# Optimization experiments

Measured on AMD Instinct MI355X. Metric: run time of the kernel, lower is better.

Reference implementation:

```python
import jax, jax.numpy as jnp
import numpy as np

B, C, W, H = 8, 256, 128, 128
CR = C // 8  # squeeze channels
EPS = 1e-5   # InstanceNorm2d default eps


def _dw_conv(x, w, b, dil):
    # depthwise 3x3 dilated conv, NCHW, kernel [C,1,3,3], 'same' padding = dil
    out = jax.lax.conv_general_dilated(
        x, w, window_strides=(1, 1),
        padding=[(dil, dil), (dil, dil)],
        rhs_dilation=(dil, dil),
        dimension_numbers=("NCHW", "OIHW", "NCHW"),
        feature_group_count=x.shape[1])
    return out + b[None, :, None, None]


def setup_inputs() -> dict:
    key = jax.random.key(0)
    ks = jax.random.split(key, 9)
    s = 0.1
    return {
        "x": jax.random.normal(ks[0], (B, C, W, H), jnp.float32),
        "wq": jax.random.normal(ks[1], (C, 1, 3, 3), jnp.float32) * s,
        "bq": jax.random.normal(ks[2], (C,), jnp.float32) * s,
        "wk": jax.random.normal(ks[3], (C, 1, 3, 3), jnp.float32) * s,
        "bk": jax.random.normal(ks[4], (C,), jnp.float32) * s,
        "w_sq": jax.random.normal(ks[5], (CR, C), jnp.float32) * s,
        "b_sq": jax.random.normal(ks[6], (CR,), jnp.float32) * s,
        "w_ex": jax.random.normal(ks[7], (C, CR), jnp.float32) * s,
        "b_ex": jax.random.normal(ks[8], (C,), jnp.float32) * s,
    }


def reference(x, wq, bq, wk, bk, w_sq, b_sq, w_ex, b_ex):
    b, c, w, h = x.shape
    q = _dw_conv(x, wq, bq, 3)   # [B,C,W,H], dilation 3
    k = _dw_conv(x, wk, bk, 6)   # [B,C,W,H], dilation 6
    # per-channel QK matmul: contracts q's last dim with k's second-to-last (requires W==H)
    attn = jnp.einsum("bcij,bcjk->bcik", q, k)  # [B,C,W,H]
    # softmax over flattened spatial dims per (b, c)
    attn = jax.nn.softmax(attn.reshape(b, c, w * h), axis=-1).reshape(b, c, w, h)
    # channel global average pool of key, broadcast-multiply
    pool = jnp.mean(k, axis=(2, 3), keepdims=True)  # [B,C,1,1]
    y = attn * pool
    # 1x1 squeeze conv C -> C//8
    s = jnp.einsum("bcwh,dc->bdwh", y, w_sq) + b_sq[None, :, None, None]
    # InstanceNorm2d (no affine, biased variance over spatial dims)
    mu = jnp.mean(s, axis=(2, 3), keepdims=True)
    var = jnp.var(s, axis=(2, 3), keepdims=True)
    s = jax.nn.relu((s - mu) * jax.lax.rsqrt(var + EPS))
    # 1x1 expand conv C//8 -> C
    out = jnp.einsum("bdwh,cd->bcwh", s, w_ex) + b_ex[None, :, None, None]
    return out
```

## Files before the change

### kernel.cpp

```cpp
#include <hip/hip_runtime.h>
#include <cstdint>

#define WDIM 128
#define NPX  16384
#define XSTR 132
#define QSTR 136
#define XPAD 16
#define LDS_A_BYTES 69888

typedef __attribute__((ext_vector_type(8))) short short8;
typedef __attribute__((ext_vector_type(4))) float f32x4;

__device__ __forceinline__ float wave_max(float v) {
#pragma unroll
  for (int m = 32; m >= 1; m >>= 1) v = fmaxf(v, __shfl_xor(v, m));
  return v;
}
__device__ __forceinline__ float wave_sum(float v) {
#pragma unroll
  for (int m = 32; m >= 1; m >>= 1) v += __shfl_xor(v, m);
  return v;
}
__device__ __forceinline__ unsigned short f2bf(float f) {
  uint32_t u = __float_as_uint(f);
  return (unsigned short)((u + 0x7fff + ((u >> 16) & 1)) >> 16);
}
__device__ __forceinline__ float bf2f(unsigned short h) {
  return __uint_as_float(((uint32_t)h) << 16);
}

template <int DIL>
__device__ __forceinline__ void dw_conv32(float* acc, const float* xq, int r,
                                          int cl, const float* w9) {
#pragma unroll
  for (int dr = 0; dr < 3; ++dr) {
    int rr = r + DIL * (dr - 1);
    if ((unsigned)rr < 128u) {
      const float* rp = &xq[rr * XSTR];
#pragma unroll
      for (int dc = 0; dc < 3; ++dc) {
        float wgt = w9[dr * 3 + dc];
        const int off = DIL * (dc - 1);
#pragma unroll
        for (int i = 0; i < 32; ++i) {
          int cc = cl + 4 * i + off;
          float v = rp[cc];
          if (i <= 1 || i >= 30) v = ((unsigned)cc < 128u) ? v : 0.f;
          acc[i] = fmaf(wgt, v, acc[i]);
        }
      }
    }
  }
}

__global__ __launch_bounds__(512, 4)
void kA(const float* __restrict__ x, const float* __restrict__ wq,
        const float* __restrict__ bq, const float* __restrict__ wk,
        const float* __restrict__ bk, unsigned short* __restrict__ y) {
  extern __shared__ char smem[];
  float* xq = (float*)smem + XPAD;
  unsigned short* qb = (unsigned short*)smem;
  unsigned short* kt = (unsigned short*)(smem + 34816);
  float* red = (float*)(smem + 69632);

  const int bc = blockIdx.x;
  const int t = threadIdx.x;
  const float* __restrict__ xp = x + (size_t)bc * NPX;

#pragma unroll
  for (int it = 0; it < 8; ++it) {
    int i = (t + it * 512) * 4;
    int r = i >> 7, c = i & 127;
    *(float4*)&xq[r * XSTR + c] = *(const float4*)&xp[i];
  }

  const int ch = bc & 255;
  float wq9[9], wk9[9];
#pragma unroll
  for (int i = 0; i < 9; ++i) { wq9[i] = wq[ch * 9 + i]; wk9[i] = wk[ch * 9 + i]; }
  const float bqv = bq[ch], bkv = bk[ch];
  __syncthreads();

  const int r = t >> 2, cl = t & 3;
  float aq[32], ak[32];
#pragma unroll
  for (int i = 0; i < 32; ++i) { aq[i] = bqv; ak[i] = bkv; }
  dw_conv32<3>(aq, xq, r, cl, wq9);
  dw_conv32<6>(ak, xq, r, cl, wk9);

  float psum = 0.f;
#pragma unroll
  for (int i = 0; i < 32; ++i) psum += ak[i];

  __syncthreads();

#pragma unroll
  for (int i = 0; i < 32; ++i) {
    int c = cl + 4 * i;
    qb[r * QSTR + c] = f2bf(aq[i]);
    kt[c * QSTR + r] = f2bf(ak[i]);
  }
  __syncthreads();

  const int w = t >> 6, lane = t & 63;
  const int wr = w >> 2, wc = w & 3;
  const int r16 = lane & 15, kg = lane >> 4;
  f32x4 acc[4][2];
#pragma unroll
  for (int mi = 0; mi < 4; ++mi)
#pragma unroll
    for (int ni = 0; ni < 2; ++ni) acc[mi][ni] = (f32x4){0.f, 0.f, 0.f, 0.f};

#pragma unroll
  for (int kk = 0; kk < 4; ++kk) {
    const int kb = kk * 32 + kg * 8;
    short8 a0 = *(const short8*)&qb[(wr * 64 + 0 * 16 + r16) * QSTR + kb];
    short8 a1 = *(const short8*)&qb[(wr * 64 + 1 * 16 + r16) * QSTR + kb];
    short8 a2 = *(const short8*)&qb[(wr * 64 + 2 * 16 + r16) * QSTR + kb];
    short8 a3 = *(const short8*)&qb[(wr * 64 + 3 * 16 + r16) * QSTR + kb];
    short8 b0 = *(const short8*)&kt[(wc * 32 + 0 + r16) * QSTR + kb];
    short8 b1 = *(const short8*)&kt[(wc * 32 + 16 + r16) * QSTR + kb];
    acc[0][0] = __builtin_amdgcn_mfma_f32_16x16x32_bf16(a0, b0, acc[0][0], 0, 0, 0);
    acc[0][1] = __builtin_amdgcn_mfma_f32_16x16x32_bf16(a0, b1, acc[0][1], 0, 0, 0);
    acc[1][0] = __builtin_amdgcn_mfma_f32_16x16x32_bf16(a1, b0, acc[1][0], 0, 0, 0);
    acc[1][1] = __builtin_amdgcn_mfma_f32_16x16x32_bf16(a1, b1, acc[1][1], 0, 0, 0);
    acc[2][0] = __builtin_amdgcn_mfma_f32_16x16x32_bf16(a2, b0, acc[2][0], 0, 0, 0);
    acc[2][1] = __builtin_amdgcn_mfma_f32_16x16x32_bf16(a2, b1, acc[2][1], 0, 0, 0);
    acc[3][0] = __builtin_amdgcn_mfma_f32_16x16x32_bf16(a3, b0, acc[3][0], 0, 0, 0);
    acc[3][1] = __builtin_amdgcn_mfma_f32_16x16x32_bf16(a3, b1, acc[3][1], 0, 0, 0);
  }

  float amax = -3.402823466e38f;
#pragma unroll
  for (int mi = 0; mi < 4; ++mi)
#pragma unroll
    for (int ni = 0; ni < 2; ++ni)
#pragma unroll
      for (int j = 0; j < 4; ++j) amax = fmaxf(amax, acc[mi][ni][j]);
  amax = wave_max(amax);
  if (lane == 0) red[w] = amax;
  __syncthreads();
  float bmax = red[0];
#pragma unroll
  for (int w2 = 1; w2 < 8; ++w2) bmax = fmaxf(bmax, red[w2]);

  float es = 0.f;
#pragma unroll
  for (int mi = 0; mi < 4; ++mi)
#pragma unroll
    for (int ni = 0; ni < 2; ++ni)
#pragma unroll
      for (int j = 0; j < 4; ++j) {
        float e = __expf(acc[mi][ni][j] - bmax);
        acc[mi][ni][j] = e;
        es += e;
      }
  es = wave_sum(es);
  float ps = wave_sum(psum);
  if (lane == 0) { red[8 + w] = es; red[16 + w] = ps; }
  __syncthreads();
  float tsum = 0.f, tpool = 0.f;
#pragma unroll
  for (int w2 = 0; w2 < 8; ++w2) { tsum += red[8 + w2]; tpool += red[16 + w2]; }
  const float scale = (tpool * (1.f / 16384.f)) / tsum;

  unsigned short* __restrict__ yp = y + (size_t)bc * NPX;
#pragma unroll
  for (int mi = 0; mi < 4; ++mi)
#pragma unroll
    for (int ni = 0; ni < 2; ++ni) {
      const int col = wc * 32 + ni * 16 + r16;
#pragma unroll
      for (int j = 0; j < 4; ++j) {
        const int row = wr * 64 + mi * 16 + kg * 4 + j;
        yp[row * WDIM + col] = f2bf(acc[mi][ni][j] * scale);
      }
    }
}

__global__ __launch_bounds__(256, 2)
void kS(const unsigned short* __restrict__ y, const float* __restrict__ w_sq,
        unsigned short* __restrict__ sT, float* __restrict__ partials) {
  __shared__ unsigned short yT[64][264];
  __shared__ float red[256];
  const int t = threadIdx.x;
  const int w = t >> 6, lane = t & 63;
  const int r16 = lane & 15, kg = lane >> 4;
  const int b = blockIdx.x >> 6;
  const int chunk = blockIdx.x & 63;
  const unsigned short* __restrict__ yb = y + (size_t)b * 256 * NPX;

  short8 aw[2][8];
#pragma unroll
  for (int mt = 0; mt < 2; ++mt)
#pragma unroll
    for (int ks = 0; ks < 8; ++ks) {
      const float* p = &w_sq[(mt * 16 + r16) * 256 + ks * 32 + kg * 8];
      float4 f0 = *(const float4*)p;
      float4 f1 = *(const float4*)(p + 4);
      short8 a;
      a[0] = f2bf(f0.x); a[1] = f2bf(f0.y); a[2] = f2bf(f0.z); a[3] = f2bf(f0.w);
      a[4] = f2bf(f1.x); a[5] = f2bf(f1.y); a[6] = f2bf(f1.z); a[7] = f2bf(f1.w);
      aw[mt][ks] = a;
    }

  float ssum[8], ssq[8];
#pragma unroll
  for (int i = 0; i < 8; ++i) { ssum[i] = 0.f; ssq[i] = 0.f; }

  for (int st = 0; st < 4; ++st) {
    const int p0 = chunk * 256 + st * 64;
#pragma unroll
    for (int it = 0; it < 8; ++it) {
      const int tid = it * 4 + w;
      const int cg = tid & 3, pg = tid >> 2;
      const int c = cg * 64 + lane;
      short8 v = *(const short8*)&yb[(size_t)c * NPX + p0 + pg * 8];
#pragma unroll
      for (int j = 0; j < 8; ++j) yT[pg * 8 + j][c] = (unsigned short)v[j];
    }
    __syncthreads();

    f32x4 acc[2][4];
#pragma unroll
    for (int mi = 0; mi < 2; ++mi)
#pragma unroll
      for (int ni = 0; ni < 4; ++ni) acc[mi][ni] = (f32x4){0.f, 0.f, 0.f, 0.f};

#pragma unroll
    for (int ks = 0; ks < 8; ++ks) {
#pragma unroll
      for (int ni = 0; ni < 4; ++ni) {
        short8 bv = *(const short8*)&yT[ni * 16 + r16][ks * 32 + kg * 8];
        acc[0][ni] = __builtin_amdgcn_mfma_f32_16x16x32_bf16(aw[0][ks], bv, acc[0][ni], 0, 0, 0);
        acc[1][ni] = __builtin_amdgcn_mfma_f32_16x16x32_bf16(aw[1][ks], bv, acc[1][ni], 0, 0, 0);
      }
    }

#pragma unroll
    for (int mi = 0; mi < 2; ++mi)
#pragma unroll
      for (int ni = 0; ni < 4; ++ni) {
        const int px = p0 + ni * 16 + r16;
        ushort4 pk;
#pragma unroll
        for (int j = 0; j < 4; ++j) {
          float v = acc[mi][ni][j];
          ssum[mi * 4 + j] += v;
          ssq[mi * 4 + j] += v * v;
          ((unsigned short*)&pk)[j] = f2bf(v);
        }
        *(ushort4*)&sT[((size_t)b * NPX + px) * 32 + mi * 16 + kg * 4] = pk;
      }
    __syncthreads();
  }

#pragma unroll
  for (int i = 0; i < 8; ++i) {
    float sm = ssum[i], sq = ssq[i];
#pragma unroll
    for (int m = 8; m >= 1; m >>= 1) {
      sm += __shfl_xor(sm, m);
      sq += __shfl_xor(sq, m);
    }
    if (r16 == 0) {
      const int d = (i >> 2) * 16 + kg * 4 + (i & 3);
      red[w * 64 + d] = sm;
      red[w * 64 + 32 + d] = sq;
    }
  }
  __syncthreads();
  if (t < 64) {
    float tot = red[t] + red[64 + t] + red[128 + t] + red[192 + t];
    partials[(size_t)blockIdx.x * 64 + t] = tot;
  }
}

__global__ void kR(const float* __restrict__ partials, float* __restrict__ mu_rs) {
  const int b = blockIdx.x, d = threadIdx.x;
  float sm = 0.f, sq = 0.f;
  for (int ch = 0; ch < 64; ++ch) {
    const float* pp = &partials[(size_t)(b * 64 + ch) * 64];
    sm += pp[d];
    sq += pp[32 + d];
  }
  float m = sm * (1.f / 16384.f);
  float v = sq * (1.f / 16384.f) - m * m;
  mu_rs[b * 64 + d] = m;
  mu_rs[b * 64 + 32 + d] = rsqrtf(v + 1e-5f);
}

__global__ __launch_bounds__(256, 3)
void kO(const unsigned short* __restrict__ sT, const float* __restrict__ mu_rs,
        const float* __restrict__ w_ex, const float* __restrict__ b_ex,
        float* __restrict__ out) {
  const int t = threadIdx.x;
  const int w = t >> 6, lane = t & 63;
  const int r16 = lane & 15, kg = lane >> 4;
  const int b = blockIdx.x >> 8;
  const int p0 = (blockIdx.x & 255) * 64;
  const int c0 = w * 64;

  short8 aw[4];
  float bex[4];
#pragma unroll
  for (int mt = 0; mt < 4; ++mt) {
    const int c = c0 + mt * 16 + r16;
    const float* p = &w_ex[c * 32 + kg * 8];
    float4 f0 = *(const float4*)p;
    float4 f1 = *(const float4*)(p + 4);
    short8 a;
    a[0] = f2bf(f0.x); a[1] = f2bf(f0.y); a[2] = f2bf(f0.z); a[3] = f2bf(f0.w);
    a[4] = f2bf(f1.x); a[5] = f2bf(f1.y); a[6] = f2bf(f1.z); a[7] = f2bf(f1.w);
    aw[mt] = a;
    bex[mt] = b_ex[c0 + mt * 16 + kg * 4];
  }

  float m8[8], r8[8];
  {
    const float* mp = &mu_rs[b * 64 + kg * 8];
    const float* rp = &mu_rs[b * 64 + 32 + kg * 8];
#pragma unroll
    for (int q = 0; q < 8; ++q) { m8[q] = mp[q]; r8[q] = rp[q]; }
  }

  f32x4 acc[4][4];
#pragma unroll
  for (int mt = 0; mt < 4; ++mt)
#pragma unroll
    for (int ni = 0; ni < 4; ++ni) acc[mt][ni] = (f32x4){0.f, 0.f, 0.f, 0.f};

#pragma unroll
  for (int ni = 0; ni < 4; ++ni) {
    const int px = p0 + ni * 16 + r16;
    short8 sv = *(const short8*)&sT[((size_t)b * NPX + px) * 32 + kg * 8];
    short8 hb;
#pragma unroll
    for (int q = 0; q < 8; ++q) {
      float f = bf2f((unsigned short)sv[q]);
      float h = fmaxf((f - m8[q]) * r8[q], 0.f);
      hb[q] = f2bf(h);
    }
#pragma unroll
    for (int mt = 0; mt < 4; ++mt)
      acc[mt][ni] = __builtin_amdgcn_mfma_f32_16x16x32_bf16(aw[mt], hb, acc[mt][ni], 0, 0, 0);
  }

  float* __restrict__ ob = out + (size_t)b * 256 * NPX;
#pragma unroll
  for (int mt = 0; mt < 4; ++mt) {
#pragma unroll
    for (int j = 0; j < 4; ++j) {
      const int c = c0 + mt * 16 + kg * 4 + j;
      const float bv = b_ex[c];
#pragma unroll
      for (int ni = 0; ni < 4; ++ni) {
        const int px = p0 + ni * 16 + r16;
        ob[(size_t)c * NPX + px] = acc[mt][ni][j] + bv;
      }
    }
  }
}

extern "C" void kernel_launch(void* const* d_in, const int* in_sizes, int n_in,
                              void* d_out, int out_size, void* d_ws, size_t ws_size,
                              hipStream_t stream) {
  (void)in_sizes; (void)n_in; (void)out_size; (void)ws_size;
  const float* x    = (const float*)d_in[0];
  const float* wq   = (const float*)d_in[1];
  const float* bq   = (const float*)d_in[2];
  const float* wk   = (const float*)d_in[3];
  const float* bk   = (const float*)d_in[4];
  const float* w_sq = (const float*)d_in[5];
  const float* w_ex = (const float*)d_in[7];
  const float* b_ex = (const float*)d_in[8];
  float* out = (float*)d_out;

  unsigned short* sT = (unsigned short*)d_ws;
  float* partials = (float*)((char*)d_ws + (size_t)8 * NPX * 32 * 2);
  float* mu_rs = partials + (size_t)512 * 64;

  unsigned short* ybf = (unsigned short*)d_out;

  hipFuncSetAttribute((const void*)kA, hipFuncAttributeMaxDynamicSharedMemorySize,
                      LDS_A_BYTES);

  kA<<<2048, 512, LDS_A_BYTES, stream>>>(x, wq, bq, wk, bk, ybf);
  kS<<<512, 256, 0, stream>>>(ybf, w_sq, sT, partials);
  kR<<<8, 32, 0, stream>>>(partials, mu_rs);
  kO<<<2048, 256, 0, stream>>>(sT, mu_rs, w_ex, b_ex, out);
}
```

Measured before the change: 131.6 us.

## Restructure depthwise conv to contiguous per-thread column windows with vector LDS loads

The depthwise conv changes from strided columns (cl+4i) to each thread owning a contiguous 32-column span, processed in two halves of 16. Each input row window is loaded once with float4 LDS reads and shared across the q and k taps that use the same row, and edge masking is applied to the whole window. Weights are forced into scalar registers via readfirstlane, and q results are written to LDS as packed short8 stores. This cuts scalar LDS load count and the per-element bounds checks, at the cost of a larger live register window and possible bank conflicts on the transposed k stores.

Result: slower. 148.5 us (+12.8%).

```diff
diff --git a/kernel.cpp b/kernel.cpp
--- a/kernel.cpp
+++ b/kernel.cpp
@@ -28,29 +28,29 @@
 __device__ __forceinline__ float bf2f(unsigned short h) {
   return __uint_as_float(((uint32_t)h) << 16);
 }
-
-template <int DIL>
-__device__ __forceinline__ void dw_conv32(float* acc, const float* xq, int r,
-                                          int cl, const float* w9) {
-#pragma unroll
-  for (int dr = 0; dr < 3; ++dr) {
-    int rr = r + DIL * (dr - 1);
-    if ((unsigned)rr < 128u) {
-      const float* rp = &xq[rr * XSTR];
-#pragma unroll
-      for (int dc = 0; dc < 3; ++dc) {
-        float wgt = w9[dr * 3 + dc];
-        const int off = DIL * (dc - 1);
-#pragma unroll
-        for (int i = 0; i < 32; ++i) {
-          int cc = cl + 4 * i + off;
-          float v = rp[cc];
-          if (i <= 1 || i >= 30) v = ((unsigned)cc < 128u) ? v : 0.f;
-          acc[i] = fmaf(wgt, v, acc[i]);
-        }
-      }
-    }
-  }
+__device__ __forceinline__ float sgpr_f(float v) {
+  return __uint_as_float(__builtin_amdgcn_readfirstlane(__float_as_uint(v)));
+}
+
+__device__ __forceinline__ void load_win(float* xw, const float* xq, int rr,
+                                         int c0h, bool mlo, bool mhi) {
+  const float* bp = &xq[rr * XSTR + c0h - 8];
+#pragma unroll
+  for (int k = 0; k < 8; ++k) *(float4*)&xw[4 * k] = *(const float4*)&bp[4 * k];
+  if (mlo) {
+#pragma unroll
+    for (int j = 0; j < 8; ++j) xw[j] = 0.f;
+  }
+  if (mhi) {
+#pragma unroll
+    for (int j = 24; j < 32; ++j) xw[j] = 0.f;
+  }
+}
+
+template <int OFF>
+__device__ __forceinline__ void tap16(float* acc, const float* xw, float w) {
+#pragma unroll
+  for (int i = 0; i < 16; ++i) acc[i] = fmaf(w, xw[8 + OFF + i], acc[i]);
 }
 
 __global__ __launch_bounds__(512, 4)
@@ -70,23 +70,55 @@
 #pragma unroll
   for (int it = 0; it < 8; ++it) {
     int i = (t + it * 512) * 4;
-    int r = i >> 7, c = i & 127;
-    *(float4*)&xq[r * XSTR + c] = *(const float4*)&xp[i];
+    int rr = i >> 7, c = i & 127;
+    *(float4*)&xq[rr * XSTR + c] = *(const float4*)&xp[i];
   }
 
   const int ch = bc & 255;
-  float wq9[9], wk9[9];
-#pragma unroll
-  for (int i = 0; i < 9; ++i) { wq9[i] = wq[ch * 9 + i]; wk9[i] = wk[ch * 9 + i]; }
-  const float bqv = bq[ch], bkv = bk[ch];
-  __syncthreads();
-
-  const int r = t >> 2, cl = t & 3;
+  float q9[9], k9[9];
+#pragma unroll
+  for (int i = 0; i < 9; ++i) {
+    q9[i] = sgpr_f(wq[ch * 9 + i]);
+    k9[i] = sgpr_f(wk[ch * 9 + i]);
+  }
+  const float bqv = sgpr_f(bq[ch]), bkv = sgpr_f(bk[ch]);
+  __syncthreads();
+
+  const int r = t >> 2, cb = t & 3;
   float aq[32], ak[32];
 #pragma unroll
   for (int i = 0; i < 32; ++i) { aq[i] = bqv; ak[i] = bkv; }
-  dw_conv32<3>(aq, xq, r, cl, wq9);
-  dw_conv32<6>(ak, xq, r, cl, wk9);
+
+#pragma unroll
+  for (int h = 0; h < 2; ++h) {
+    const int c0h = cb * 32 + h * 16;
+    const bool mlo = (cb == 0) && (h == 0);
+    const bool mhi = (cb == 3) && (h == 1);
+    float* aqh = aq + h * 16;
+    float* akh = ak + h * 16;
+    float xw[32];
+    if (r >= 6) {
+      load_win(xw, xq, r - 6, c0h, mlo, mhi);
+      tap16<-6>(akh, xw, k9[0]); tap16<0>(akh, xw, k9[1]); tap16<6>(akh, xw, k9[2]);
+    }
+    if (r >= 3) {
+      load_win(xw, xq, r - 3, c0h, mlo, mhi);
+      tap16<-3>(aqh, xw, q9[0]); tap16<0>(aqh, xw, q9[1]); tap16<3>(aqh, xw, q9[2]);
+    }
+    {
+      load_win(xw, xq, r, c0h, mlo, mhi);
+      tap16<-3>(aqh, xw, q9[3]); tap16<0>(aqh, xw, q9[4]); tap16<3>(aqh, xw, q9[5]);
+      tap16<-6>(akh, xw, k9[3]); tap16<0>(akh, xw, k9[4]); tap16<6>(akh, xw, k9[5]);
+    }
+    if (r < 125) {
+      load_win(xw, xq, r + 3, c0h, mlo, mhi);
+      tap16<-3>(aqh, xw, q9[6]); tap16<0>(aqh, xw, q9[7]); tap16<3>(aqh, xw, q9[8]);
+    }
+    if (r < 122) {
+      load_win(xw, xq, r + 6, c0h, mlo, mhi);
+      tap16<-6>(akh, xw, k9[6]); tap16<0>(akh, xw, k9[7]); tap16<6>(akh, xw, k9[8]);
+    }
+  }
 
   float psum = 0.f;
 #pragma unroll
@@ -95,11 +127,14 @@
   __syncthreads();
 
 #pragma unroll
-  for (int i = 0; i < 32; ++i) {
-    int c = cl + 4 * i;
-    qb[r * QSTR + c] = f2bf(aq[i]);
-    kt[c * QSTR + r] = f2bf(ak[i]);
-  }
+  for (int g = 0; g < 4; ++g) {
+    short8 pk;
+#pragma unroll
+    for (int j = 0; j < 8; ++j) pk[j] = (short)f2bf(aq[g * 8 + j]);
+    *(short8*)&qb[r * QSTR + cb * 32 + g * 8] = pk;
+  }
+#pragma unroll
+  for (int i = 0; i < 32; ++i) kt[(cb * 32 + i) * QSTR + r] = f2bf(ak[i]);
   __syncthreads();
 
   const int w = t >> 6, lane = t & 63;
@@ -302,7 +337,6 @@
   const int c0 = w * 64;
 
   short8 aw[4];
-  float bex[4];
 #pragma unroll
   for (int mt = 0; mt < 4; ++mt) {
     const int c = c0 + mt * 16 + r16;
@@ -313,7 +347,6 @@
     a[0] = f2bf(f0.x); a[1] = f2bf(f0.y); a[2] = f2bf(f0.z); a[3] = f2bf(f0.w);
     a[4] = f2bf(f1.x); a[5] = f2bf(f1.y); a[6] = f2bf(f1.z); a[7] = f2bf(f1.w);
     aw[mt] = a;
-    bex[mt] = b_ex[c0 + mt * 16 + kg * 4];
   }
 
   float m8[8], r8[8];
```
